# Kernel optimization log

Measured on AMD Instinct MI355X. Metric: run time of the kernel, lower is better.

The kernel has to match this reference:

```python
import jax, jax.numpy as jnp
import numpy as np

N_NODES = 100000
N_EDGES = 1600000
IN_DIM = 128
HID2 = 128   # hidden_dim * 2
OUT_DIM = 1


def setup_inputs() -> dict:
    key = jax.random.key(0)
    ks = jax.random.split(key, 9)
    x = jax.random.normal(ks[0], (N_NODES, IN_DIM), dtype=jnp.float32)
    edge_index = jax.random.randint(ks[1], (2, N_EDGES), 0, N_NODES, dtype=jnp.int32)
    s_in = 1.0 / np.sqrt(IN_DIM)
    s_h = 1.0 / np.sqrt(HID2)
    W_conv = jax.random.normal(ks[2], (IN_DIM, HID2), dtype=jnp.float32) * s_in
    b_conv = jnp.zeros((HID2,), dtype=jnp.float32)
    W_proj = jax.random.normal(ks[3], (IN_DIM, HID2), dtype=jnp.float32) * s_in
    b_proj = jax.random.normal(ks[4], (HID2,), dtype=jnp.float32) * s_in
    W_out = jax.random.normal(ks[5], (HID2, OUT_DIM), dtype=jnp.float32) * s_h
    b_out = jax.random.normal(ks[6], (OUT_DIM,), dtype=jnp.float32) * s_h
    return {"x": x, "edge_index": edge_index, "W_conv": W_conv, "b_conv": b_conv,
            "W_proj": W_proj, "b_proj": b_proj, "W_out": W_out, "b_out": b_out}


def reference(x, edge_index, W_conv, b_conv, W_proj, b_proj, W_out, b_out):
    n = x.shape[0]
    loops = jnp.arange(n, dtype=edge_index.dtype)
    self_loops = jnp.stack([loops, loops])  # [2, N]
    # self loops added twice: once in forward() explicitly, once inside GCNConv (default)
    ei = jnp.concatenate([edge_index, self_loops, self_loops], axis=1)
    row, col = ei[0], ei[1]  # source -> destination
    # symmetric GCN normalization: deg computed over destinations
    deg = jax.ops.segment_sum(jnp.ones_like(row, dtype=x.dtype), col, num_segments=n)
    dinv = jnp.where(deg > 0, deg ** -0.5, 0.0)
    norm = dinv[row] * dinv[col]  # [E']
    xw = x @ W_conv  # [N, HID2]
    msgs = xw[row] * norm[:, None]  # [E', HID2] gather + scale
    conv = jax.ops.segment_sum(msgs, col, num_segments=n) + b_conv
    combined = jax.nn.relu(conv + x @ W_proj + b_proj)
    out = combined @ W_out + b_out  # [N, 1]
    return out.squeeze()
```

## Files before the change

kernel.cpp:

```cpp
#include <hip/hip_runtime.h>

#define N_NODES 100000
#define N_EDGES 1600000
#define DIM 128
#define NBIN 128
#define WINSZ 782
#define SLOT 64
#define CH 4096
#define NP1 ((N_EDGES + CH - 1) / CH)
#define SUBCAP 80
#define NGEMM ((N_NODES + 63) / 64)
#define SENT 0xFFFFFFFFu

typedef __attribute__((ext_vector_type(8))) short short8;
typedef __attribute__((ext_vector_type(4))) float f32x4;

__device__ inline unsigned short bf16u(float f) {
    unsigned u = __builtin_bit_cast(unsigned, f);
    return (unsigned short)((u + 0x7FFFu + ((u >> 16) & 1u)) >> 16);
}
__device__ inline unsigned pk_bf16(float a, float b) {
    return (unsigned)bf16u(a) | ((unsigned)bf16u(b) << 16);
}
__device__ inline float bf16_lo(unsigned v) { return __builtin_bit_cast(float, v << 16); }
__device__ inline float bf16_hi(unsigned v) { return __builtin_bit_cast(float, v & 0xFFFF0000u); }

__device__ inline unsigned pk_fp8x4(float a, float b, float c, float d) {
    int lo = __builtin_amdgcn_cvt_pk_fp8_f32(a, b, 0, false);
    int hi = __builtin_amdgcn_cvt_pk_fp8_f32(c, d, lo, true);
    return (unsigned)hi;
}
__device__ inline float fp8_b0(int v) { return __builtin_amdgcn_cvt_f32_fp8(v, 0); }
__device__ inline float fp8_b1(int v) { return __builtin_amdgcn_cvt_f32_fp8(v, 1); }


__launch_bounds__(256)
__global__ void k_prep(const float* __restrict__ Wc, const float* __restrict__ Wp,
                       const int* __restrict__ erow, const int* __restrict__ ecol,
                       int* __restrict__ cntT, unsigned* __restrict__ gbin,
                       unsigned short* __restrict__ WtG) {
    const int tid = threadIdx.x;
    if (blockIdx.x >= NP1) {
        int idx = (blockIdx.x - NP1) * 256 + tid;
        int n = idx >> 7, k = idx & 127;
        float v = (n < 128) ? Wc[k * 128 + n] : Wp[k * 128 + (n - 128)];
        int t = n >> 4, mm = n & 15;
        int q = k >> 5, qd = (k >> 3) & 3, j = k & 7;
        WtG[(((t * 4 + q) * 64 + qd * 16 + mm) << 3) + j] = bf16u(v);
        return;
    }
    __shared__ int lcnt[NBIN];
    const int blk = blockIdx.x;
    if (tid < NBIN) lcnt[tid] = 0;
    __syncthreads();
    const int e0 = blk * CH;
    const int e1 = (e0 + CH < N_EDGES) ? e0 + CH : N_EDGES;
    for (int e = e0 + tid; e < e1; e += 256) {
        int c = ecol[e];
        int bin = c / WINSZ;
        unsigned pay = (unsigned)erow[e] | ((unsigned)(c - bin * WINSZ) << 17);
        int r = atomicAdd(&lcnt[bin], 1);
        if (r < SUBCAP) gbin[((size_t)bin * NP1 + blk) * SUBCAP + r] = pay;
    }
    __syncthreads();
    if (tid < NBIN) {
        int v = lcnt[tid];
        cntT[blk * NBIN + tid] = (v < SUBCAP) ? v : SUBCAP;
    }
}

__launch_bounds__(256)
__global__ void k_bins(const int* __restrict__ cntT,
                       const unsigned* __restrict__ gbin,
                       int* __restrict__ srcb2,
                       int* __restrict__ cnt,
                       float* __restrict__ dinv) {
    __shared__ int lcnt[WINSZ];
    __shared__ int cl[NP1];
    const int tid = threadIdx.x;
    const int bin = blockIdx.x;
    const int lo  = bin * WINSZ;
    const int nw  = (lo + WINSZ < N_NODES) ? WINSZ : (N_NODES - lo);
    if (nw <= 0) return;
    for (int i = tid; i < WINSZ; i += 256) lcnt[i] = 0;
    for (int i = tid; i < NP1; i += 256) cl[i] = cntT[i * NBIN + bin];
    __syncthreads();

    const int wv = tid >> 6, ln = tid & 63;
    const int g = wv * 2 + (ln >> 5);
    const int lidx = ln & 31;
    const size_t binbase = (size_t)bin * NP1 * SUBCAP;

    int sg = g;
    int len = cl[sg];
    const unsigned* seg = gbin + binbase + (size_t)sg * SUBCAP;
    unsigned p0 = (lidx < len) ? seg[lidx] : SENT;
    unsigned p1 = (lidx + 32 < len) ? seg[lidx + 32] : SENT;

    while (sg < NP1) {
        const int nsg = sg + 8;
        int nlen = 0;
        const unsigned* nseg = seg;
        unsigned n0 = SENT, n1 = SENT;
        if (nsg < NP1) {
            nlen = cl[nsg];
            nseg = gbin + binbase + (size_t)nsg * SUBCAP;
            n0 = (lidx < nlen) ? nseg[lidx] : SENT;
            n1 = (lidx + 32 < nlen) ? nseg[lidx + 32] : SENT;
        }
        if (p0 != SENT) {
            int row = p0 & 0x1FFFF, c = p0 >> 17;
            int r = atomicAdd(&lcnt[c], 1);
            if (r < SLOT) srcb2[(lo + c) * SLOT + r] = row;
        }
        if (p1 != SENT) {
            int row = p1 & 0x1FFFF, c = p1 >> 17;
            int r = atomicAdd(&lcnt[c], 1);
            if (r < SLOT) srcb2[(lo + c) * SLOT + r] = row;
        }
        if (len > 64) {
            for (int i = lidx + 64; i < len; i += 32) {
                unsigned pay = seg[i];
                int row = pay & 0x1FFFF, c = pay >> 17;
                int r = atomicAdd(&lcnt[c], 1);
                if (r < SLOT) srcb2[(lo + c) * SLOT + r] = row;
            }
        }
        sg = nsg; len = nlen; seg = nseg; p0 = n0; p1 = n1;
    }
    __syncthreads();
    for (int i = tid; i < nw; i += 256) {
        int v = lcnt[i];
        cnt[lo + i]  = (v < SLOT) ? v : SLOT;
        dinv[lo + i] = rsqrtf((float)(v + 2));
    }
}

__global__ void k_gemm(const float* __restrict__ x,
                       const unsigned short* __restrict__ WtG,
                       const float* __restrict__ bc,
                       const float* __restrict__ bp,
                       const float* __restrict__ dinv,
                       unsigned* __restrict__ xwb8,
                       unsigned* __restrict__ accb) {
    __shared__ alignas(16) unsigned short wbuf[16384];

    const int tid   = threadIdx.x;
    const int node0 = blockIdx.x * 64;
    const int w     = tid >> 6;
    const int lane  = tid & 63;
    const int m     = lane & 15;
    const int quad  = lane >> 4;

    const uint4* gsrc = (const uint4*)WtG;
    uint4*       lbuf = (uint4*)wbuf;

    #pragma unroll
    for (int i = 0; i < 8; ++i) lbuf[i * 256 + tid] = gsrc[i * 256 + tid];

    const int  rowg  = node0 + w * 16 + m;
    const bool valid = rowg < N_NODES;
    const float* xrow = x + (size_t)rowg * DIM;

    short8 afr[4];
    #pragma unroll
    for (int q = 0; q < 4; q++) {
        float4 xa = make_float4(0.f, 0.f, 0.f, 0.f);
        float4 xb = make_float4(0.f, 0.f, 0.f, 0.f);
        if (valid) {
            xa = *(const float4*)(xrow + 32 * q + 8 * quad);
            xb = *(const float4*)(xrow + 32 * q + 8 * quad + 4);
        }
        uint4 pa;
        pa.x = pk_bf16(xa.x, xa.y); pa.y = pk_bf16(xa.z, xa.w);
        pa.z = pk_bf16(xb.x, xb.y); pa.w = pk_bf16(xb.z, xb.w);
        afr[q] = __builtin_bit_cast(short8, pa);
    }

    float bias[8];
    #pragma unroll
    for (int p = 0; p < 4; p++) {
        bias[2 * p]     = bc[32 * p + m]      + bp[32 * p + m];
        bias[2 * p + 1] = bc[32 * p + m + 16] + bp[32 * p + m + 16];
    }

    __syncthreads();

    f32x4 acc0[8];
    #pragma unroll
    for (int t = 0; t < 8; ++t) {
        f32x4 a = (f32x4){0.f, 0.f, 0.f, 0.f};
        #pragma unroll
        for (int q = 0; q < 4; ++q) {
            short8 bfrag = *(const short8*)(wbuf + (((t * 4 + q) * 64 + lane) << 3));
            a = __builtin_amdgcn_mfma_f32_16x16x32_bf16(afr[q], bfrag, a, 0, 0, 0);
        }
        acc0[t] = a;
    }

    #pragma unroll
    for (int r = 0; r < 4; ++r) {
        int node = node0 + w * 16 + quad * 4 + r;
        if (node < N_NODES) {
            float dv = dinv[node];
            uint2 xv;
            xv.x = pk_fp8x4(acc0[0][r] * dv, acc0[1][r] * dv,
                            acc0[2][r] * dv, acc0[3][r] * dv);
            xv.y = pk_fp8x4(acc0[4][r] * dv, acc0[5][r] * dv,
                            acc0[6][r] * dv, acc0[7][r] * dv);
            *(uint2*)(xwb8 + (size_t)node * 32 + m * 2) = xv;
        }
    }

    __syncthreads();

    #pragma unroll
    for (int i = 0; i < 8; ++i) lbuf[i * 256 + tid] = gsrc[2048 + i * 256 + tid];

    __syncthreads();

    f32x4 acc1[8];
    #pragma unroll
    for (int t = 0; t < 8; ++t) {
        f32x4 a = (f32x4){0.f, 0.f, 0.f, 0.f};
        #pragma unroll
        for (int q = 0; q < 4; ++q) {
            short8 bfrag = *(const short8*)(wbuf + (((t * 4 + q) * 64 + lane) << 3));
            a = __builtin_amdgcn_mfma_f32_16x16x32_bf16(afr[q], bfrag, a, 0, 0, 0);
        }
        acc1[t] = a;
    }

    #pragma unroll
    for (int r = 0; r < 4; ++r) {
        int node = node0 + w * 16 + quad * 4 + r;
        if (node < N_NODES) {
            uint4 pv;
            pv.x = pk_bf16(acc1[0][r] + bias[0], acc1[1][r] + bias[1]);
            pv.y = pk_bf16(acc1[2][r] + bias[2], acc1[3][r] + bias[3]);
            pv.z = pk_bf16(acc1[4][r] + bias[4], acc1[5][r] + bias[5]);
            pv.w = pk_bf16(acc1[6][r] + bias[6], acc1[7][r] + bias[7]);
            *(uint4*)(accb + (size_t)node * 64 + m * 4) = pv;
        }
    }
}

__launch_bounds__(256)
__global__ void k_gather_final(const int* __restrict__ srcb2,
                               const int* __restrict__ cnt,
                               const float* __restrict__ dinv,
                               const unsigned short* __restrict__ xw8,
                               const unsigned* __restrict__ accb,
                               const float* __restrict__ wout,
                               const float* __restrict__ bout,
                               float* __restrict__ out) {
    int t = blockIdx.x * 256 + threadIdx.x;
    int node = t >> 6;
    unsigned lane = (unsigned)(t & 63);
    if (node >= N_NODES) return;

    int c = cnt[node];
    const int* sp = srcb2 + node * SLOT;
    float ddst = dinv[node];

    unsigned av = accb[(unsigned)node * 64u + lane];
    float px = bf16_lo(av);
    float py = bf16_hi(av);

    int vs = xw8[((unsigned)node << 6) | lane];
    float sx = 2.0f * fp8_b0(vs), sy = 2.0f * fp8_b1(vs);
    float tx = 0.f, ty = 0.f;

    int j = 0;
    for (; j + 8 <= c; j += 8) {
        int4 ra = *(const int4*)(sp + j);
        int4 rb = *(const int4*)(sp + j + 4);
        int v0 = xw8[((unsigned)ra.x << 6) | lane];
        int v1 = xw8[((unsigned)ra.y << 6) | lane];
        int v2 = xw8[((unsigned)ra.z << 6) | lane];
        int v3 = xw8[((unsigned)ra.w << 6) | lane];
        int v4 = xw8[((unsigned)rb.x << 6) | lane];
        int v5 = xw8[((unsigned)rb.y << 6) | lane];
        int v6 = xw8[((unsigned)rb.z << 6) | lane];
        int v7 = xw8[((unsigned)rb.w << 6) | lane];
        sx += fp8_b0(v0) + fp8_b0(v1) + fp8_b0(v2) + fp8_b0(v3);
        sy += fp8_b1(v0) + fp8_b1(v1) + fp8_b1(v2) + fp8_b1(v3);
        tx += fp8_b0(v4) + fp8_b0(v5) + fp8_b0(v6) + fp8_b0(v7);
        ty += fp8_b1(v4) + fp8_b1(v5) + fp8_b1(v6) + fp8_b1(v7);
    }
    if (j < c) {
        const int mx = c - 1;
        int i1 = j + 1, i2 = j + 2, i3 = j + 3;
        int i4 = j + 4, i5 = j + 5, i6 = j + 6, i7 = j + 7;
        int r0 = sp[j];
        int r1 = sp[(i1 < mx) ? i1 : mx], r2 = sp[(i2 < mx) ? i2 : mx];
        int r3 = sp[(i3 < mx) ? i3 : mx], r4 = sp[(i4 < mx) ? i4 : mx];
        int r5 = sp[(i5 < mx) ? i5 : mx], r6 = sp[(i6 < mx) ? i6 : mx];
        int r7 = sp[(i7 < mx) ? i7 : mx];
        int v0 = xw8[((unsigned)r0 << 6) | lane];
        int v1 = xw8[((unsigned)r1 << 6) | lane];
        int v2 = xw8[((unsigned)r2 << 6) | lane];
        int v3 = xw8[((unsigned)r3 << 6) | lane];
        int v4 = xw8[((unsigned)r4 << 6) | lane];
        int v5 = xw8[((unsigned)r5 << 6) | lane];
        int v6 = xw8[((unsigned)r6 << 6) | lane];
        int v7 = xw8[((unsigned)r7 << 6) | lane];
        v1 = (i1 < c) ? v1 : 0;  v2 = (i2 < c) ? v2 : 0;
        v3 = (i3 < c) ? v3 : 0;  v4 = (i4 < c) ? v4 : 0;
        v5 = (i5 < c) ? v5 : 0;  v6 = (i6 < c) ? v6 : 0;
        v7 = (i7 < c) ? v7 : 0;
        sx += fp8_b0(v0) + fp8_b0(v1) + fp8_b0(v2) + fp8_b0(v3);
        sy += fp8_b1(v0) + fp8_b1(v1) + fp8_b1(v2) + fp8_b1(v3);
        tx += fp8_b0(v4) + fp8_b0(v5) + fp8_b0(v6) + fp8_b0(v7);
        ty += fp8_b1(v4) + fp8_b1(v5) + fp8_b1(v6) + fp8_b1(v7);
    }
    float ax = px + ddst * (sx + tx);
    float ay = py + ddst * (sy + ty);

    int f0 = 32 * (lane & 3) + (lane >> 2);
    float w0 = wout[f0], w1 = wout[f0 + 16];
    float s = fmaxf(ax, 0.f) * w0 + fmaxf(ay, 0.f) * w1;
    #pragma unroll
    for (int off = 32; off > 0; off >>= 1) s += __shfl_down(s, off);
    if (lane == 0) out[node] = s + bout[0];
}

extern "C" void kernel_launch(void* const* d_in, const int* in_sizes, int n_in,
                              void* d_out, int out_size, void* d_ws, size_t ws_size,
                              hipStream_t stream) {
    const float* x      = (const float*)d_in[0];
    const int*   ei     = (const int*)  d_in[1];
    const float* W_conv = (const float*)d_in[2];
    const float* b_conv = (const float*)d_in[3];
    const float* W_proj = (const float*)d_in[4];
    const float* b_proj = (const float*)d_in[5];
    const float* W_out  = (const float*)d_in[6];
    const float* b_out  = (const float*)d_in[7];
    float* out = (float*)d_out;

    const int* e_row = ei;
    const int* e_col = ei + N_EDGES;

    char* p = (char*)d_ws;
    unsigned*       xwb8  = (unsigned*)p;       p += (size_t)N_NODES * 32 * 4;
    unsigned*       accb  = (unsigned*)p;       p += (size_t)N_NODES * 64 * 4;
    int*            srcb2 = (int*)p;            p += (size_t)N_NODES * SLOT * 4;
    unsigned*       gbin  = (unsigned*)p;       p += (size_t)NBIN * NP1 * SUBCAP * 4;
    int*            cntT  = (int*)p;            p += (size_t)NP1 * NBIN * 4;
    int*            cnt   = (int*)p;            p += (size_t)N_NODES * 4;
    float*          dinv  = (float*)p;          p += (size_t)N_NODES * 4;
    unsigned short* WtG   = (unsigned short*)p; p += 256 * 128 * 2;

    k_prep<<<NP1 + 128, 256, 0, stream>>>(W_conv, W_proj, e_row, e_col, cntT, gbin, WtG);
    k_bins<<<NBIN, 256, 0, stream>>>(cntT, gbin, srcb2, cnt, dinv);
    k_gemm<<<NGEMM, 256, 0, stream>>>(x, WtG, b_conv, b_proj, dinv, xwb8, accb);
    k_gather_final<<<(N_NODES * 64 + 255) / 256, 256, 0, stream>>>(
        srcb2, cnt, dinv, (const unsigned short*)xwb8, accb, W_out, b_out, out);
}
```

Baseline: 211.1 us.

## Gather 4 fp8 features per lane with half-wave edge split; transpose gbin layout

The gather kernel now has each lane load a 32-bit word holding four fp8 features instead of a 16-bit pair. The two half-waves handle alternating edges and combine through a cross-half shuffle, and decoding uses packed fp8-to-f32 conversion. Separately, the binning staging buffer is laid out block-major rather than bin-major, so each prep block writes to contiguous memory. Together these aim to cut per-edge load instructions and improve write locality, at the cost of an extra shuffle step and a changed feature-to-lane mapping that the output weights must match.

```diff
diff --git a/kernel.cpp b/kernel.cpp
--- a/kernel.cpp
+++ b/kernel.cpp
@@ -14,6 +14,7 @@
 
 typedef __attribute__((ext_vector_type(8))) short short8;
 typedef __attribute__((ext_vector_type(4))) float f32x4;
+typedef __attribute__((ext_vector_type(2))) float f32x2;
 
 __device__ inline unsigned short bf16u(float f) {
     unsigned u = __builtin_bit_cast(unsigned, f);
@@ -30,8 +31,28 @@
     int hi = __builtin_amdgcn_cvt_pk_fp8_f32(c, d, lo, true);
     return (unsigned)hi;
 }
-__device__ inline float fp8_b0(int v) { return __builtin_amdgcn_cvt_f32_fp8(v, 0); }
-__device__ inline float fp8_b1(int v) { return __builtin_amdgcn_cvt_f32_fp8(v, 1); }
+
+#if __has_builtin(__builtin_amdgcn_cvt_pk_f32_fp8)
+__device__ inline f32x2 pkcvt_lo(unsigned v) {
+    return __builtin_amdgcn_cvt_pk_f32_fp8(v, false);
+}
+__device__ inline f32x2 pkcvt_hi(unsigned v) {
+    return __builtin_amdgcn_cvt_pk_f32_fp8(v, true);
+}
+#else
+__device__ inline f32x2 pkcvt_lo(unsigned v) {
+    f32x2 r;
+    r.x = __builtin_amdgcn_cvt_f32_fp8((int)v, 0);
+    r.y = __builtin_amdgcn_cvt_f32_fp8((int)v, 1);
+    return r;
+}
+__device__ inline f32x2 pkcvt_hi(unsigned v) {
+    f32x2 r;
+    r.x = __builtin_amdgcn_cvt_f32_fp8((int)v, 2);
+    r.y = __builtin_amdgcn_cvt_f32_fp8((int)v, 3);
+    return r;
+}
+#endif
 
 
 __launch_bounds__(256)
@@ -60,7 +81,7 @@
         int bin = c / WINSZ;
         unsigned pay = (unsigned)erow[e] | ((unsigned)(c - bin * WINSZ) << 17);
         int r = atomicAdd(&lcnt[bin], 1);
-        if (r < SUBCAP) gbin[((size_t)bin * NP1 + blk) * SUBCAP + r] = pay;
+        if (r < SUBCAP) gbin[((size_t)blk * NBIN + bin) * SUBCAP + r] = pay;
     }
     __syncthreads();
     if (tid < NBIN) {
@@ -89,11 +110,10 @@
     const int wv = tid >> 6, ln = tid & 63;
     const int g = wv * 2 + (ln >> 5);
     const int lidx = ln & 31;
-    const size_t binbase = (size_t)bin * NP1 * SUBCAP;
 
     int sg = g;
     int len = cl[sg];
-    const unsigned* seg = gbin + binbase + (size_t)sg * SUBCAP;
+    const unsigned* seg = gbin + ((size_t)sg * NBIN + bin) * SUBCAP;
     unsigned p0 = (lidx < len) ? seg[lidx] : SENT;
     unsigned p1 = (lidx + 32 < len) ? seg[lidx + 32] : SENT;
 
@@ -104,7 +124,7 @@
         unsigned n0 = SENT, n1 = SENT;
         if (nsg < NP1) {
             nlen = cl[nsg];
-            nseg = gbin + binbase + (size_t)nsg * SUBCAP;
+            nseg = gbin + ((size_t)nsg * NBIN + bin) * SUBCAP;
             n0 = (lidx < nlen) ? nseg[lidx] : SENT;
             n1 = (lidx + 32 < nlen) ? nseg[lidx + 32] : SENT;
         }
@@ -249,80 +269,89 @@
 __global__ void k_gather_final(const int* __restrict__ srcb2,
                                const int* __restrict__ cnt,
                                const float* __restrict__ dinv,
-                               const unsigned short* __restrict__ xw8,
+                               const unsigned* __restrict__ xw32,
                                const unsigned* __restrict__ accb,
                                const float* __restrict__ wout,
                                const float* __restrict__ bout,
                                float* __restrict__ out) {
     int t = blockIdx.x * 256 + threadIdx.x;
     int node = t >> 6;
-    unsigned lane = (unsigned)(t & 63);
+    int lane = t & 63;
     if (node >= N_NODES) return;
 
+    const int d  = lane & 31;
+    const int eh = lane >> 5;
     int c = cnt[node];
     const int* sp = srcb2 + node * SLOT;
     float ddst = dinv[node];
 
-    unsigned av = accb[(unsigned)node * 64u + lane];
-    float px = bf16_lo(av);
-    float py = bf16_hi(av);
-
-    int vs = xw8[((unsigned)node << 6) | lane];
-    float sx = 2.0f * fp8_b0(vs), sy = 2.0f * fp8_b1(vs);
-    float tx = 0.f, ty = 0.f;
+    f32x2 a01 = (f32x2){0.f, 0.f};
+    f32x2 a23 = (f32x2){0.f, 0.f};
 
     int j = 0;
     for (; j + 8 <= c; j += 8) {
         int4 ra = *(const int4*)(sp + j);
         int4 rb = *(const int4*)(sp + j + 4);
-        int v0 = xw8[((unsigned)ra.x << 6) | lane];
-        int v1 = xw8[((unsigned)ra.y << 6) | lane];
-        int v2 = xw8[((unsigned)ra.z << 6) | lane];
-        int v3 = xw8[((unsigned)ra.w << 6) | lane];
-        int v4 = xw8[((unsigned)rb.x << 6) | lane];
-        int v5 = xw8[((unsigned)rb.y << 6) | lane];
-        int v6 = xw8[((unsigned)rb.z << 6) | lane];
-        int v7 = xw8[((unsigned)rb.w << 6) | lane];
-        sx += fp8_b0(v0) + fp8_b0(v1) + fp8_b0(v2) + fp8_b0(v3);
-        sy += fp8_b1(v0) + fp8_b1(v1) + fp8_b1(v2) + fp8_b1(v3);
-        tx += fp8_b0(v4) + fp8_b0(v5) + fp8_b0(v6) + fp8_b0(v7);
-        ty += fp8_b1(v4) + fp8_b1(v5) + fp8_b1(v6) + fp8_b1(v7);
+        int r0 = eh ? ra.y : ra.x;
+        int r1 = eh ? ra.w : ra.z;
+        int r2 = eh ? rb.y : rb.x;
+        int r3 = eh ? rb.w : rb.z;
+        unsigned v0 = xw32[((unsigned)r0 << 5) | d];
+        unsigned v1 = xw32[((unsigned)r1 << 5) | d];
+        unsigned v2 = xw32[((unsigned)r2 << 5) | d];
+        unsigned v3 = xw32[((unsigned)r3 << 5) | d];
+        a01 += pkcvt_lo(v0); a23 += pkcvt_hi(v0);
+        a01 += pkcvt_lo(v1); a23 += pkcvt_hi(v1);
+        a01 += pkcvt_lo(v2); a23 += pkcvt_hi(v2);
+        a01 += pkcvt_lo(v3); a23 += pkcvt_hi(v3);
     }
     if (j < c) {
         const int mx = c - 1;
-        int i1 = j + 1, i2 = j + 2, i3 = j + 3;
-        int i4 = j + 4, i5 = j + 5, i6 = j + 6, i7 = j + 7;
-        int r0 = sp[j];
-        int r1 = sp[(i1 < mx) ? i1 : mx], r2 = sp[(i2 < mx) ? i2 : mx];
-        int r3 = sp[(i3 < mx) ? i3 : mx], r4 = sp[(i4 < mx) ? i4 : mx];
-        int r5 = sp[(i5 < mx) ? i5 : mx], r6 = sp[(i6 < mx) ? i6 : mx];
-        int r7 = sp[(i7 < mx) ? i7 : mx];
-        int v0 = xw8[((unsigned)r0 << 6) | lane];
-        int v1 = xw8[((unsigned)r1 << 6) | lane];
-        int v2 = xw8[((unsigned)r2 << 6) | lane];
-        int v3 = xw8[((unsigned)r3 << 6) | lane];
-        int v4 = xw8[((unsigned)r4 << 6) | lane];
-        int v5 = xw8[((unsigned)r5 << 6) | lane];
-        int v6 = xw8[((unsigned)r6 << 6) | lane];
-        int v7 = xw8[((unsigned)r7 << 6) | lane];
-        v1 = (i1 < c) ? v1 : 0;  v2 = (i2 < c) ? v2 : 0;
-        v3 = (i3 < c) ? v3 : 0;  v4 = (i4 < c) ? v4 : 0;
-        v5 = (i5 < c) ? v5 : 0;  v6 = (i6 < c) ? v6 : 0;
-        v7 = (i7 < c) ? v7 : 0;
-        sx += fp8_b0(v0) + fp8_b0(v1) + fp8_b0(v2) + fp8_b0(v3);
-        sy += fp8_b1(v0) + fp8_b1(v1) + fp8_b1(v2) + fp8_b1(v3);
-        tx += fp8_b0(v4) + fp8_b0(v5) + fp8_b0(v6) + fp8_b0(v7);
-        ty += fp8_b1(v4) + fp8_b1(v5) + fp8_b1(v6) + fp8_b1(v7);
-    }
-    float ax = px + ddst * (sx + tx);
-    float ay = py + ddst * (sy + ty);
-
-    int f0 = 32 * (lane & 3) + (lane >> 2);
-    float w0 = wout[f0], w1 = wout[f0 + 16];
-    float s = fmaxf(ax, 0.f) * w0 + fmaxf(ay, 0.f) * w1;
-    #pragma unroll
-    for (int off = 32; off > 0; off >>= 1) s += __shfl_down(s, off);
-    if (lane == 0) out[node] = s + bout[0];
+        int p0 = j + eh, p1 = j + 2 + eh, p2 = j + 4 + eh, p3 = j + 6 + eh;
+        int r0 = sp[(p0 < mx) ? p0 : mx];
+        int r1 = sp[(p1 < mx) ? p1 : mx];
+        int r2 = sp[(p2 < mx) ? p2 : mx];
+        int r3 = sp[(p3 < mx) ? p3 : mx];
+        unsigned v0 = xw32[((unsigned)r0 << 5) | d];
+        unsigned v1 = xw32[((unsigned)r1 << 5) | d];
+        unsigned v2 = xw32[((unsigned)r2 << 5) | d];
+        unsigned v3 = xw32[((unsigned)r3 << 5) | d];
+        if (p0 >= c) v0 = 0u;
+        if (p1 >= c) v1 = 0u;
+        if (p2 >= c) v2 = 0u;
+        if (p3 >= c) v3 = 0u;
+        a01 += pkcvt_lo(v0); a23 += pkcvt_hi(v0);
+        a01 += pkcvt_lo(v1); a23 += pkcvt_hi(v1);
+        a01 += pkcvt_lo(v2); a23 += pkcvt_hi(v2);
+        a01 += pkcvt_lo(v3); a23 += pkcvt_hi(v3);
+    }
+
+    a01.x += __shfl_down(a01.x, 32);
+    a01.y += __shfl_down(a01.y, 32);
+    a23.x += __shfl_down(a23.x, 32);
+    a23.y += __shfl_down(a23.y, 32);
+
+    unsigned vs = xw32[((unsigned)node << 5) | d];
+    f32x2 sl0 = pkcvt_lo(vs), sl1 = pkcvt_hi(vs);
+    float s0 = a01.x + 2.f * sl0.x;
+    float s1 = a01.y + 2.f * sl0.y;
+    float s2 = a23.x + 2.f * sl1.x;
+    float s3 = a23.y + 2.f * sl1.y;
+
+    uint2 av = *(const uint2*)(accb + ((unsigned)node << 6) + 2u * d);
+    float v0 = bf16_lo(av.x) + ddst * s0;
+    float v1 = bf16_hi(av.x) + ddst * s1;
+    float v2 = bf16_lo(av.y) + ddst * s2;
+    float v3 = bf16_hi(av.y) + ddst * s3;
+
+    int f00 = 64 * (d & 1) + (d >> 1);
+    float r = fmaxf(v0, 0.f) * wout[f00]
+            + fmaxf(v1, 0.f) * wout[f00 + 16]
+            + fmaxf(v2, 0.f) * wout[f00 + 32]
+            + fmaxf(v3, 0.f) * wout[f00 + 48];
+    #pragma unroll
+    for (int off = 16; off > 0; off >>= 1) r += __shfl_down(r, off);
+    if (lane == 0) out[node] = r + bout[0];
 }
 
 extern "C" void kernel_launch(void* const* d_in, const int* in_sizes, int n_in,
@@ -355,5 +384,5 @@
     k_bins<<<NBIN, 256, 0, stream>>>(cntT, gbin, srcb2, cnt, dinv);
     k_gemm<<<NGEMM, 256, 0, stream>>>(x, WtG, b_conv, b_proj, dinv, xwb8, accb);
     k_gather_final<<<(N_NODES * 64 + 255) / 256, 256, 0, stream>>>(
-        srcb2, cnt, dinv, (const unsigned short*)xwb8, accb, W_out, b_out, out);
-}
+        srcb2, cnt, dinv, xwb8, accb, W_out, b_out, out);
+}
```

New measurement: 212.4 us. No clear change (+0.6%).
